# Performance work log

Measured on AMD Instinct MI355X. Metric: run time of the kernel, lower is better.

The kernel has to match this reference:

```python
import jax, jax.numpy as jnp
import numpy as np

H = 4096       # hidden_size
D_IN = 8192    # intermediate_size
N = 16         # ssm_state_size
K = 4          # conv_kernel
R = 256        # time_step_rank
EPS = 1e-6     # mixer_rms_eps


def rms_forward(x, eps=EPS):
    xf = x.astype(jnp.float32)
    var = jnp.mean(xf * xf, axis=-1, keepdims=True)
    return (xf * jax.lax.rsqrt(var + eps)).astype(x.dtype)


def setup_inputs() -> dict:
    key = jax.random.key(0)
    ks = jax.random.split(key, 10)
    s = 0.02
    hidden_states = jax.random.normal(ks[0], (2, 1024, H), dtype=jnp.float32)
    W_in = jax.random.normal(ks[1], (2 * D_IN, H), dtype=jnp.float32) * s
    conv_w = jax.random.normal(ks[2], (D_IN, K), dtype=jnp.float32) * 0.2
    conv_b = jax.random.normal(ks[3], (D_IN,), dtype=jnp.float32) * 0.02
    W_x = jax.random.normal(ks[4], (R + 2 * N, D_IN), dtype=jnp.float32) * s
    W_dt = jax.random.normal(ks[5], (D_IN, R), dtype=jnp.float32) * s
    b_dt = jax.random.normal(ks[6], (D_IN,), dtype=jnp.float32) * 0.02
    A_log = jnp.log(jnp.broadcast_to(jnp.arange(1, N + 1, dtype=jnp.float32)[None, :], (D_IN, N)))
    D = jnp.ones((D_IN,), dtype=jnp.float32)
    W_out = jax.random.normal(ks[7], (H, D_IN), dtype=jnp.float32) * s
    return {"hidden_states": hidden_states, "W_in": W_in, "conv_w": conv_w,
            "conv_b": conv_b, "W_x": W_x, "W_dt": W_dt, "b_dt": b_dt,
            "A_log": A_log, "D": D, "W_out": W_out}


def reference(hidden_states, W_in, conv_w, conv_b, W_x, W_dt, b_dt, A_log, D, W_out):
    b, L, _ = hidden_states.shape
    # in_proj -> split into x and gate  [b, L, d_in] each
    proj = hidden_states @ W_in.T
    x, gate = proj[..., :D_IN], proj[..., D_IN:]
    # depthwise causal conv1d over time (padding K-1, keep first L) + SiLU
    xpad = jnp.pad(x, ((0, 0), (K - 1, 0), (0, 0)))
    xc = conv_b
    for j in range(K):
        xc = xc + conv_w[:, j] * xpad[:, j:j + L, :]
    x = jax.nn.silu(xc)                               # [b, L, d_in]
    # x_proj -> dt / B / C, each RMS-normalized (weightless, FalconMamba)
    ssm = x @ W_x.T                                   # [b, L, R+2N]
    ts, Bm, Cm = ssm[..., :R], ssm[..., R:R + N], ssm[..., R + N:]
    ts = rms_forward(ts)
    Bm = rms_forward(Bm)
    Cm = rms_forward(Cm)
    dt = jax.nn.softplus(ts @ W_dt.T + b_dt)          # [b, L, d_in]
    A = -jnp.exp(A_log.astype(jnp.float32))           # [d_in, N]
    # selective scan over time: state [b, d_in, N]
    def step(state, inp):
        dt_t, B_t, C_t, u_t = inp                     # [b,d],[b,N],[b,N],[b,d]
        dA = jnp.exp(dt_t[..., None] * A)             # [b, d_in, N]
        state = state * dA + (dt_t * u_t)[..., None] * B_t[:, None, :]
        y = jnp.einsum('bdn,bn->bd', state, C_t)
        return state, y
    init = jnp.zeros((b, D_IN, N), dtype=jnp.float32)
    xs = (dt.transpose(1, 0, 2), Bm.transpose(1, 0, 2),
          Cm.transpose(1, 0, 2), x.transpose(1, 0, 2))
    _, ys = jax.lax.scan(step, init, xs)              # [L, b, d_in]
    y = ys.transpose(1, 0, 2) + x * D                 # skip with D
    y = y * jax.nn.silu(gate)                         # gated output
    return y @ W_out.T                                # [b, L, H]
```

## Files before the change

kernel.cpp:

```cpp
#include <hip/hip_runtime.h>
#include <hip/hip_bf16.h>

#define DIN 8192
#define HH 4096
#define BLT 2048
#define LSEQ 1024
#define CL 64
#define NCG 32

typedef unsigned short u16;
typedef __bf16 bf16x8 __attribute__((ext_vector_type(8)));
typedef float f32x4v __attribute__((ext_vector_type(4)));

__device__ __forceinline__ u16 f2b(float f) {
  unsigned u = __float_as_uint(f);
  u += 0x7fff + ((u >> 16) & 1);
  return (u16)(u >> 16);
}
__device__ __forceinline__ float b2f(u16 h) {
  return __uint_as_float(((unsigned)h) << 16);
}

__device__ __forceinline__ void gl_lds16(const u16* g, u16* l) {
  __builtin_amdgcn_global_load_lds(
      (const __attribute__((address_space(1))) void*)g,
      (__attribute__((address_space(3))) void*)l, 16, 0, 0);
}

__device__ __forceinline__ int bsw(int r) { return (r & 3) ^ ((r >> 2) & 3); }

__global__ void cvt_in_kernel(const float* __restrict__ Win, u16* __restrict__ Winb,
                              const float* __restrict__ hs, u16* __restrict__ hsb) {
  const long stride = (long)gridDim.x * blockDim.x * 4;
  const long base = ((long)blockIdx.x * blockDim.x + threadIdx.x) * 4;
  for (long i = base; i < 67108864L; i += stride) {
    f32x4v v = *(const f32x4v*)(Win + i);
    ushort4 o;
    o.x = f2b(v[0]); o.y = f2b(v[1]); o.z = f2b(v[2]); o.w = f2b(v[3]);
    *(ushort4*)(Winb + i) = o;
  }
  for (long i = base; i < 8388608L; i += stride) {
    f32x4v v = *(const f32x4v*)(hs + i);
    ushort4 o;
    o.x = f2b(v[0]); o.y = f2b(v[1]); o.z = f2b(v[2]); o.w = f2b(v[3]);
    *(ushort4*)(hsb + i) = o;
  }
}

__global__ void cvt_weights_kernel(
    const float* __restrict__ Wout, u16* __restrict__ Woutb,
    const float* __restrict__ Wdt, u16* __restrict__ Wdtb,
    const float* __restrict__ Wx, u16* __restrict__ Wxb)
{
  const long stride = (long)gridDim.x * blockDim.x * 4;
  const long base = ((long)blockIdx.x * blockDim.x + threadIdx.x) * 4;
  for (long i = base; i < 33554432L; i += stride) {
    f32x4v v = *(const f32x4v*)(Wout + i);
    ushort4 o;
    o.x = f2b(v[0]); o.y = f2b(v[1]); o.z = f2b(v[2]); o.w = f2b(v[3]);
    *(ushort4*)(Woutb + i) = o;
  }
  for (long i = base; i < 2097152L; i += stride) {
    f32x4v v = *(const f32x4v*)(Wdt + i);
    ushort4 o;
    o.x = f2b(v[0]); o.y = f2b(v[1]); o.z = f2b(v[2]); o.w = f2b(v[3]);
    *(ushort4*)(Wdtb + i) = o;
  }
  for (long i = base; i < (long)512 * DIN; i += stride) {
    ushort4 o;
    if (i < (long)288 * DIN) {
      f32x4v v = *(const f32x4v*)(Wx + i);
      o.x = f2b(v[0]); o.y = f2b(v[1]); o.z = f2b(v[2]); o.w = f2b(v[3]);
    } else {
      o.x = 0; o.y = 0; o.z = 0; o.w = 0;
    }
    *(ushort4*)(Wxb + i) = o;
  }
}

__global__ void add2_kernel(const float* __restrict__ a, const float* __restrict__ b,
                            float* __restrict__ o, long n) {
  long i = ((long)blockIdx.x * blockDim.x + threadIdx.x) * 4;
  long stride = (long)gridDim.x * blockDim.x * 4;
  for (; i < n; i += stride) {
    f32x4v va = *(const f32x4v*)(a + i);
    f32x4v vb = *(const f32x4v*)(b + i);
    *(f32x4v*)(o + i) = va + vb;
  }
}

template<int MODE>
__global__ __launch_bounds__(512, 2) void gemm256(
    const u16* __restrict__ A, const u16* __restrict__ B, void* __restrict__ Cp,
    int M, int N, int Kfull, int Ksub, const float* __restrict__ bias = nullptr)
{
  __shared__ __align__(16) u16 lds[3][2][8192];
  const int tid = threadIdx.x;
  const int lane = tid & 63;
  const int wid = tid >> 6;
  const int wm = wid >> 2;
  const int wn = wid & 3;
  const int fr = lane & 15;
  const int fq = lane >> 4;
  const int fs = fq ^ bsw(fr);

  const int nbx = N >> 8;
  const int cpx = gridDim.x >> 3;
  const int bid = blockIdx.x;
  const int swz = (bid & 7) * cpx + (bid >> 3);
  const long m0 = (long)(swz / nbx) << 8;
  const long n0 = (long)(swz % nbx) << 8;
  const long kbase = (long)blockIdx.y * Ksub;

  const int srow = tid >> 2;
  const int sseg = (tid & 3) ^ bsw(srow);
  const u16* ag0 = A + (m0 + srow) * (long)Kfull + kbase + sseg * 8;
  const u16* ag1 = ag0 + 128 * (long)Kfull;
  const u16* bg0 = B + (n0 + srow) * (long)Kfull + kbase + sseg * 8;
  const u16* bg1 = bg0 + 128 * (long)Kfull;

  auto stageA = [&](int c, int koff) {
    gl_lds16(ag0 + koff, &lds[c][0][tid * 8]);
    gl_lds16(bg0 + koff, &lds[c][1][tid * 8]);
  };
  auto stageB = [&](int c, int koff) {
    gl_lds16(ag1 + koff, &lds[c][0][4096 + tid * 8]);
    gl_lds16(bg1 + koff, &lds[c][1][4096 + tid * 8]);
  };

  const int NT = Ksub >> 5;
  stageA(0, 0); stageB(0, 0);
  stageA(1, 32); stageB(1, 32);
  asm volatile("s_waitcnt vmcnt(4)" ::: "memory");
  __builtin_amdgcn_s_barrier();

  f32x4v acc[8][4];
#pragma unroll
  for (int i = 0; i < 8; ++i)
#pragma unroll
    for (int j = 0; j < 4; ++j) acc[i][j] = (f32x4v){0.f, 0.f, 0.f, 0.f};

  const int aoff = (wm * 128 + fr) * 32 + fs * 8;
  const int boff = (wn * 64 + fr) * 32 + fs * 8;
  bf16x8 af[4], bfg[4], al[4];

  int c = 0, cs = 2;
  for (int t = 0; t < NT; ++t) {
    const u16* Asl = &lds[c][0][0];
    const u16* Bsl = &lds[c][1][0];
    const bool pf = (t + 2 < NT);
#pragma unroll
    for (int mi = 0; mi < 4; ++mi) af[mi] = *(const bf16x8*)(Asl + aoff + mi * 512);
#pragma unroll
    for (int ni = 0; ni < 4; ++ni) bfg[ni] = *(const bf16x8*)(Bsl + boff + ni * 512);
    if (pf) stageA(cs, (t + 2) * 32);
    __builtin_amdgcn_s_barrier();
    asm volatile("s_waitcnt lgkmcnt(0)" ::: "memory");
    __builtin_amdgcn_sched_barrier(0);
    __builtin_amdgcn_s_setprio(1);
#pragma unroll
    for (int mi = 0; mi < 4; ++mi)
#pragma unroll
      for (int ni = 0; ni < 4; ++ni)
        acc[mi][ni] = __builtin_amdgcn_mfma_f32_16x16x32_bf16(af[mi], bfg[ni], acc[mi][ni], 0, 0, 0);
    __builtin_amdgcn_s_setprio(0);
#pragma unroll
    for (int mi = 0; mi < 4; ++mi) al[mi] = *(const bf16x8*)(Asl + aoff + 2048 + mi * 512);
    if (pf) stageB(cs, (t + 2) * 32);
    __builtin_amdgcn_s_barrier();
    asm volatile("s_waitcnt lgkmcnt(0)" ::: "memory");
    __builtin_amdgcn_sched_barrier(0);
    __builtin_amdgcn_s_setprio(1);
#pragma unroll
    for (int mi = 0; mi < 4; ++mi)
#pragma unroll
      for (int ni = 0; ni < 4; ++ni)
        acc[mi + 4][ni] = __builtin_amdgcn_mfma_f32_16x16x32_bf16(al[mi], bfg[ni], acc[mi + 4][ni], 0, 0, 0);
    __builtin_amdgcn_s_setprio(0);
    if (pf) {
      asm volatile("s_waitcnt vmcnt(4)" ::: "memory");
    } else {
      asm volatile("s_waitcnt vmcnt(0)" ::: "memory");
    }
    __builtin_amdgcn_s_barrier();
    c = (c == 2) ? 0 : c + 1;
    cs = (cs == 2) ? 0 : cs + 1;
  }

  float* Cf = (float*)Cp + (size_t)blockIdx.y * M * N;
#pragma unroll
  for (int mi = 0; mi < 8; ++mi) {
#pragma unroll
    for (int ni = 0; ni < 4; ++ni) {
      const long col = n0 + wn * 64 + ni * 16 + fr;
      const long rbase = m0 + wm * 128 + mi * 16 + fq * 4;
#pragma unroll
      for (int r = 0; r < 4; ++r) {
        if constexpr (MODE == 1) {
          ((u16*)Cp)[(rbase + r) * N + col] = f2b(acc[mi][ni][r]);
        } else if constexpr (MODE == 0) {
          Cf[(rbase + r) * N + col] = acc[mi][ni][r];
        } else {
          const float z = acc[mi][ni][r] + bias[rbase + r];
          ((float*)Cp)[(rbase + r) * N + col] = (z > 20.f) ? z : log1pf(__expf(z));
        }
      }
    }
  }
}

__global__ __launch_bounds__(256) void conv_silu_tr_kernel(
    const u16* __restrict__ proj, const float* __restrict__ conv_w,
    const float* __restrict__ conv_b, u16* __restrict__ xb, u16* __restrict__ xT)
{
  __shared__ u16 xt[64][68];
  const int t = threadIdx.x;
  const int tr = t >> 4;
  const int dqi = t & 15;
  const long tok0 = (long)blockIdx.x * 64;
  const int d0 = blockIdx.y * 64;
  const int d = d0 + dqi * 4;
  f32x4v cb = *(const f32x4v*)(conv_b + d);
  f32x4v w0 = *(const f32x4v*)(conv_w + (size_t)(d + 0) * 4);
  f32x4v w1 = *(const f32x4v*)(conv_w + (size_t)(d + 1) * 4);
  f32x4v w2 = *(const f32x4v*)(conv_w + (size_t)(d + 2) * 4);
  f32x4v w3 = *(const f32x4v*)(conv_w + (size_t)(d + 3) * 4);
#pragma unroll
  for (int tt = 0; tt < 4; ++tt) {
    const long tok = tok0 + tr + tt * 16;
    const int l = (int)(tok & (LSEQ - 1));
    float a0 = cb[0], a1 = cb[1], a2 = cb[2], a3 = cb[3];
#pragma unroll
    for (int j = 0; j < 4; ++j) {
      const int lj = l - 3 + j;
      if (lj >= 0) {
        ushort4 xv = *(const ushort4*)(proj + (tok - 3 + j) * 16384 + d);
        a0 = fmaf(w0[j], b2f(xv.x), a0);
        a1 = fmaf(w1[j], b2f(xv.y), a1);
        a2 = fmaf(w2[j], b2f(xv.z), a2);
        a3 = fmaf(w3[j], b2f(xv.w), a3);
      }
    }
    ushort4 o;
    o.x = f2b(a0 / (1.f + __expf(-a0)));
    o.y = f2b(a1 / (1.f + __expf(-a1)));
    o.z = f2b(a2 / (1.f + __expf(-a2)));
    o.w = f2b(a3 / (1.f + __expf(-a3)));
    *(ushort4*)(xb + tok * DIN + d) = o;
    *(ushort4*)(&xt[tr + tt * 16][dqi * 4]) = o;
  }
  __syncthreads();
  const int dl = t >> 2;
  const int tq = t & 3;
  u16 buf[16];
#pragma unroll
  for (int i = 0; i < 16; ++i) buf[i] = xt[tq * 16 + i][dl];
  u16* dst = xT + (size_t)(d0 + dl) * BLT + tok0 + tq * 16;
  *(ushort4*)(dst + 0)  = *(ushort4*)&buf[0];
  *(ushort4*)(dst + 4)  = *(ushort4*)&buf[4];
  *(ushort4*)(dst + 8)  = *(ushort4*)&buf[8];
  *(ushort4*)(dst + 12) = *(ushort4*)&buf[12];
}

__global__ __launch_bounds__(64) void rms_kernel(
    const float* __restrict__ part, u16* __restrict__ tsb,
    float* __restrict__ Bn, float* __restrict__ Cn)
{
  const int tok = blockIdx.x;
  const int lane = threadIdx.x;
  const size_t rowoff = (size_t)tok * 512;
  f32x4v t = (f32x4v){0.f, 0.f, 0.f, 0.f};
#pragma unroll
  for (int s = 0; s < 16; ++s)
    t += *(const f32x4v*)(part + (size_t)s * (BLT * 512) + rowoff + lane * 4);
  float ss = t[0]*t[0] + t[1]*t[1] + t[2]*t[2] + t[3]*t[3];
#pragma unroll
  for (int o = 32; o; o >>= 1) ss += __shfl_xor(ss, o);
  const float sc = rsqrtf(ss * (1.f / 256.f) + 1e-6f);
  ushort4 o4;
  o4.x = f2b(t[0] * sc); o4.y = f2b(t[1] * sc);
  o4.z = f2b(t[2] * sc); o4.w = f2b(t[3] * sc);
  *(ushort4*)(tsb + (size_t)tok * 256 + lane * 4) = o4;

  float v = 0.f;
  if (lane < 32) {
#pragma unroll
    for (int s = 0; s < 16; ++s)
      v += part[(size_t)s * (BLT * 512) + rowoff + 256 + lane];
  }
  float g = v * v;
#pragma unroll
  for (int o = 1; o < 16; o <<= 1) g += __shfl_xor(g, o);
  const float scBC = rsqrtf(g * (1.f / 16.f) + 1e-6f);
  if (lane < 16) Bn[(size_t)tok * 16 + lane] = v * scBC;
  else if (lane < 32) Cn[(size_t)tok * 16 + (lane - 16)] = v * scBC;
}

__global__ __launch_bounds__(256) void scan_p1_kernel(
    const float* __restrict__ dtT, const u16* __restrict__ xT,
    const float* __restrict__ Bn, const float* __restrict__ A_log,
    float* __restrict__ partE, float* __restrict__ partS)
{
  __shared__ float Bsh[CL][16];
  const int tid = threadIdx.x;
  const int chunk = blockIdx.y;
  const int d = blockIdx.x * 64 + (tid >> 2);
  const int ln = tid & 3;
  const int tok0 = chunk * CL;
  {
    const int tt = tid >> 2, q = tid & 3;
    *(f32x4v*)&Bsh[tt][q * 4] = *(const f32x4v*)(Bn + (size_t)(tok0 + tt) * 16 + q * 4);
  }
  __syncthreads();
  float a[4];
#pragma unroll
  for (int j = 0; j < 4; ++j) a[j] = -__expf(A_log[(size_t)d * 16 + ln * 4 + j]);
  float E0 = 1.f, E1 = 1.f, E2 = 1.f, E3 = 1.f;
  float S0 = 0.f, S1 = 0.f, S2 = 0.f, S3 = 0.f;
  const float* dtp = dtT + (size_t)d * BLT + tok0;
  const u16* xp = xT + (size_t)d * BLT + tok0;
  for (int l = 0; l < CL; l += 4) {
    f32x4v dt4 = *(const f32x4v*)(dtp + l);
    ushort4 u4 = *(const ushort4*)(xp + l);
#pragma unroll
    for (int i = 0; i < 4; ++i) {
      const float dt = dt4[i];
      const float u = b2f(((const u16*)&u4)[i]);
      const float dtu = dt * u;
      f32x4v Bv = *(const f32x4v*)&Bsh[l + i][ln * 4];
      const float e0 = __expf(dt * a[0]);
      const float e1 = __expf(dt * a[1]);
      const float e2 = __expf(dt * a[2]);
      const float e3 = __expf(dt * a[3]);
      S0 = fmaf(S0, e0, dtu * Bv[0]); E0 *= e0;
      S1 = fmaf(S1, e1, dtu * Bv[1]); E1 *= e1;
      S2 = fmaf(S2, e2, dtu * Bv[2]); E2 *= e2;
      S3 = fmaf(S3, e3, dtu * Bv[3]); E3 *= e3;
    }
  }
  const size_t off = (size_t)chunk * (DIN * 16) + (size_t)d * 16 + ln * 4;
  f32x4v Ev = {E0, E1, E2, E3}, Sv = {S0, S1, S2, S3};
  *(f32x4v*)(partE + off) = Ev;
  *(f32x4v*)(partS + off) = Sv;
}

__global__ __launch_bounds__(256) void scan_p2_kernel(
    const float* __restrict__ partE, float* __restrict__ partS)
{
  const int dn = blockIdx.x * 256 + threadIdx.x;
  float s = 0.f;
  for (int c = 0; c < NCG; ++c) {
    if ((c & 15) == 0) s = 0.f;
    const size_t off = (size_t)c * (DIN * 16) + dn;
    const float e = partE[off];
    const float ps = partS[off];
    partS[off] = s;
    s = fmaf(e, s, ps);
  }
}

__global__ __launch_bounds__(256) void scan_p3_kernel(
    const float* __restrict__ dtT, const u16* __restrict__ xT,
    const float* __restrict__ Bn, const float* __restrict__ Cn,
    const float* __restrict__ A_log, const float* __restrict__ Dv,
    const float* __restrict__ stateIn, const u16* __restrict__ proj,
    u16* __restrict__ yg)
{
  __shared__ float Bsh[CL][16], Csh[CL][16];
  __shared__ u16 gsh[CL][64], ysh[CL][64];
  const int tid = threadIdx.x;
  const int chunk = blockIdx.y;
  const int d0 = blockIdx.x * 64;
  const int dch = tid >> 2;
  const int d = d0 + dch;
  const int ln = tid & 3;
  const int tok0 = chunk * CL;
  {
    const int tt = tid >> 2, q = tid & 3;
    *(f32x4v*)&Bsh[tt][q * 4] = *(const f32x4v*)(Bn + (size_t)(tok0 + tt) * 16 + q * 4);
    *(f32x4v*)&Csh[tt][q * 4] = *(const f32x4v*)(Cn + (size_t)(tok0 + tt) * 16 + q * 4);
    const u16* grow = proj + (size_t)(tok0 + tt) * 16384 + DIN + d0 + q * 16;
#pragma unroll
    for (int qq = 0; qq < 4; ++qq)
      *(ushort4*)&gsh[tt][q * 16 + qq * 4] = *(const ushort4*)(grow + qq * 4);
  }
  __syncthreads();
  float a[4];
#pragma unroll
  for (int j = 0; j < 4; ++j) a[j] = -__expf(A_log[(size_t)d * 16 + ln * 4 + j]);
  f32x4v sv = *(const f32x4v*)(stateIn + (size_t)chunk * (DIN * 16) + (size_t)d * 16 + ln * 4);
  float S0 = sv[0], S1 = sv[1], S2 = sv[2], S3 = sv[3];
  const float Dd = Dv[d];
  const float* dtp = dtT + (size_t)d * BLT + tok0;
  const u16* xp = xT + (size_t)d * BLT + tok0;
  for (int l = 0; l < CL; l += 4) {
    f32x4v dt4 = *(const f32x4v*)(dtp + l);
    ushort4 u4 = *(const ushort4*)(xp + l);
#pragma unroll
    for (int i = 0; i < 4; ++i) {
      const float dt = dt4[i];
      const float u = b2f(((const u16*)&u4)[i]);
      const float dtu = dt * u;
      f32x4v Bv = *(const f32x4v*)&Bsh[l + i][ln * 4];
      f32x4v Cv = *(const f32x4v*)&Csh[l + i][ln * 4];
      const float e0 = __expf(dt * a[0]);
      const float e1 = __expf(dt * a[1]);
      const float e2 = __expf(dt * a[2]);
      const float e3 = __expf(dt * a[3]);
      float y;
      S0 = fmaf(S0, e0, dtu * Bv[0]); y = S0 * Cv[0];
      S1 = fmaf(S1, e1, dtu * Bv[1]); y = fmaf(S1, Cv[1], y);
      S2 = fmaf(S2, e2, dtu * Bv[2]); y = fmaf(S2, Cv[2], y);
      S3 = fmaf(S3, e3, dtu * Bv[3]); y = fmaf(S3, Cv[3], y);
      y += __shfl_xor(y, 1);
      y += __shfl_xor(y, 2);
      if (ln == 0) {
        const float yt = fmaf(u, Dd, y);
        const float gt = b2f(gsh[l + i][dch]);
        const float sg = gt / (1.f + __expf(-gt));
        ysh[l + i][dch] = f2b(yt * sg);
      }
    }
  }
  __syncthreads();
  {
    const int tt = tid >> 2, q = tid & 3;
    u16* yrow = yg + (size_t)(tok0 + tt) * DIN + d0 + q * 16;
#pragma unroll
    for (int qq = 0; qq < 4; ++qq)
      *(ushort4*)(yrow + qq * 4) = *(ushort4*)&ysh[tt][q * 16 + qq * 4];
  }
}

extern "C" void kernel_launch(void* const* d_in, const int* in_sizes, int n_in,
                              void* d_out, int out_size, void* d_ws, size_t ws_size,
                              hipStream_t stream) {
  const float* hs     = (const float*)d_in[0];
  const float* W_in   = (const float*)d_in[1];
  const float* conv_w = (const float*)d_in[2];
  const float* conv_b = (const float*)d_in[3];
  const float* W_x    = (const float*)d_in[4];
  const float* W_dt   = (const float*)d_in[5];
  const float* b_dt   = (const float*)d_in[6];
  const float* A_log  = (const float*)d_in[7];
  const float* Dv     = (const float*)d_in[8];
  const float* W_out  = (const float*)d_in[9];
  float* out = (float*)d_out;

  char* ws = (char*)d_ws;
  size_t off = 0;
  auto alloc = [&](size_t bytes) -> char* {
    char* p = ws + off;
    off += (bytes + 255) & ~(size_t)255;
    return p;
  };

  u16* W_in_b = (u16*)alloc(134217728);
  u16* hs_b = (u16*)alloc(16777216);
  u16* proj_b = (u16*)alloc((size_t)BLT * 16384 * 2);
  u16* x_b    = (u16*)alloc((size_t)BLT * DIN * 2);
  u16* W_xp_b = (u16*)alloc((size_t)512 * DIN * 2);
  u16* yg_b   = (u16*)alloc((size_t)BLT * DIN * 2);
  u16* x_T    = (u16*)alloc((size_t)BLT * DIN * 2);

  float* dt_T    = (float*)W_in_b;
  float* ssm_part= (float*)W_in_b;
  u16*   W_out_b = (u16*)((char*)W_in_b + 67108864);
  u16*   ts_b    = (u16*)((char*)hs_b + 3145728);
  float* Bn      = (float*)((char*)hs_b + 3145728 + 1048576);
  float* Cn      = (float*)((char*)hs_b + 3145728 + 1048576 + 131072);
  u16*   W_dt_b  = (u16*)((char*)hs_b + 3145728 + 1048576 + 262144);
  float* partE   = (float*)x_b;
  float* partS   = (float*)((char*)x_b + 16777216);
  float* out_part= (float*)proj_b;

  const int CG = 2048;
  cvt_in_kernel<<<CG, 256, 0, stream>>>(W_in, W_in_b, hs, hs_b);
  gemm256<1><<<dim3((16384 / 256) * (BLT / 256), 1), 512, 0, stream>>>(hs_b, W_in_b, proj_b, BLT, 16384, 4096, 4096);
  cvt_weights_kernel<<<CG, 256, 0, stream>>>(W_out, W_out_b, W_dt, W_dt_b, W_x, W_xp_b);
  conv_silu_tr_kernel<<<dim3(BLT / 64, DIN / 64), 256, 0, stream>>>(proj_b, conv_w, conv_b, x_b, x_T);
  gemm256<0><<<dim3((512 / 256) * (BLT / 256), 16), 512, 0, stream>>>(x_b, W_xp_b, ssm_part, BLT, 512, DIN, DIN / 16);
  rms_kernel<<<BLT, 64, 0, stream>>>(ssm_part, ts_b, Bn, Cn);
  gemm256<2><<<dim3((DIN / 256) * (BLT / 256), 1), 512, 0, stream>>>(W_dt_b, ts_b, dt_T, DIN, BLT, 256, 256, b_dt);
  scan_p1_kernel<<<dim3(DIN / 64, NCG), 256, 0, stream>>>(dt_T, x_T, Bn, A_log, partE, partS);
  scan_p2_kernel<<<DIN * 16 / 256, 256, 0, stream>>>(partE, partS);
  scan_p3_kernel<<<dim3(DIN / 64, NCG), 256, 0, stream>>>(dt_T, x_T, Bn, Cn, A_log, Dv, partS, proj_b, yg_b);
  gemm256<0><<<dim3((HH / 256) * (BLT / 256), 2), 512, 0, stream>>>(yg_b, W_out_b, out_part, BLT, HH, DIN, DIN / 2);
  add2_kernel<<<CG, 256, 0, stream>>>(out_part, out_part + (size_t)BLT * HH, out, (long)BLT * HH);
}
```

Before: 897.5 us.

## Replace split-K output GEMM and add kernel with a 256x128 tile GEMM

The final out-projection GEMM previously used split-K=2 with 256x256 tiles, writing two fp32 partial outputs and then summing them in a separate add kernel. It is replaced by a new 256x128-tile GEMM that walks the full K dimension and writes the output directly, which gives the same 256-block grid while removing the partial-buffer traffic and one launch. The x_proj GEMM epilogue also skips storing padded columns beyond 288. The cost is a longer serial K loop per block and a smaller tile that reuses each loaded operand less.

Measured after the change: 888.6 us (median of 2 runs). No clear change (-1.0%).

```diff
diff --git a/kernel.cpp b/kernel.cpp
--- a/kernel.cpp
+++ b/kernel.cpp
@@ -78,21 +78,11 @@
   }
 }
 
-__global__ void add2_kernel(const float* __restrict__ a, const float* __restrict__ b,
-                            float* __restrict__ o, long n) {
-  long i = ((long)blockIdx.x * blockDim.x + threadIdx.x) * 4;
-  long stride = (long)gridDim.x * blockDim.x * 4;
-  for (; i < n; i += stride) {
-    f32x4v va = *(const f32x4v*)(a + i);
-    f32x4v vb = *(const f32x4v*)(b + i);
-    *(f32x4v*)(o + i) = va + vb;
-  }
-}
-
 template<int MODE>
 __global__ __launch_bounds__(512, 2) void gemm256(
     const u16* __restrict__ A, const u16* __restrict__ B, void* __restrict__ Cp,
-    int M, int N, int Kfull, int Ksub, const float* __restrict__ bias = nullptr)
+    int M, int N, int Kfull, int Ksub, const float* __restrict__ bias = nullptr,
+    int nlim = 1 << 30)
 {
   __shared__ __align__(16) u16 lds[3][2][8192];
   const int tid = threadIdx.x;
@@ -199,12 +189,103 @@
         if constexpr (MODE == 1) {
           ((u16*)Cp)[(rbase + r) * N + col] = f2b(acc[mi][ni][r]);
         } else if constexpr (MODE == 0) {
-          Cf[(rbase + r) * N + col] = acc[mi][ni][r];
+          if (col < nlim) Cf[(rbase + r) * N + col] = acc[mi][ni][r];
         } else {
           const float z = acc[mi][ni][r] + bias[rbase + r];
           ((float*)Cp)[(rbase + r) * N + col] = (z > 20.f) ? z : log1pf(__expf(z));
         }
       }
+    }
+  }
+}
+
+__global__ __launch_bounds__(512, 2) void gemm256n128(
+    const u16* __restrict__ A, const u16* __restrict__ B, float* __restrict__ Cp,
+    int M, int N, int K)
+{
+  __shared__ __align__(16) u16 lds[3][12288];
+  const int tid = threadIdx.x;
+  const int lane = tid & 63;
+  const int wid = tid >> 6;
+  const int wm = wid >> 1;
+  const int wn = wid & 1;
+  const int fr = lane & 15;
+  const int fq = lane >> 4;
+  const int fs = fq ^ bsw(fr);
+
+  const int nbx = N >> 7;
+  const int cpx = gridDim.x >> 3;
+  const int bid = blockIdx.x;
+  const int swz = (bid & 7) * cpx + (bid >> 3);
+  const long m0 = (long)(swz / nbx) << 8;
+  const long n0 = (long)(swz % nbx) << 7;
+
+  const int srow = tid >> 2;
+  const int sseg = (tid & 3) ^ bsw(srow);
+  const u16* ag0 = A + (m0 + srow) * (long)K + sseg * 8;
+  const u16* ag1 = ag0 + 128 * (long)K;
+  const u16* bg0 = B + (n0 + srow) * (long)K + sseg * 8;
+
+  auto stage = [&](int c, int koff) {
+    gl_lds16(ag0 + koff, &lds[c][tid * 8]);
+    gl_lds16(ag1 + koff, &lds[c][4096 + tid * 8]);
+    gl_lds16(bg0 + koff, &lds[c][8192 + tid * 8]);
+  };
+
+  const int NT = K >> 5;
+  stage(0, 0);
+  stage(1, 32);
+  asm volatile("s_waitcnt vmcnt(3)" ::: "memory");
+  __builtin_amdgcn_s_barrier();
+
+  f32x4v acc[4][4];
+#pragma unroll
+  for (int i = 0; i < 4; ++i)
+#pragma unroll
+    for (int j = 0; j < 4; ++j) acc[i][j] = (f32x4v){0.f, 0.f, 0.f, 0.f};
+
+  const int aoff = (wm * 64 + fr) * 32 + fs * 8;
+  const int boff = 8192 + (wn * 64 + fr) * 32 + fs * 8;
+  bf16x8 af[4], bfg[4];
+
+  int c = 0, cs = 2;
+  for (int t = 0; t < NT; ++t) {
+    const u16* L = &lds[c][0];
+    const bool pf = (t + 2 < NT);
+#pragma unroll
+    for (int mi = 0; mi < 4; ++mi) af[mi] = *(const bf16x8*)(L + aoff + mi * 512);
+#pragma unroll
+    for (int ni = 0; ni < 4; ++ni) bfg[ni] = *(const bf16x8*)(L + boff + ni * 512);
+    if (pf) stage(cs, (t + 2) * 32);
+    __builtin_amdgcn_s_barrier();
+    asm volatile("s_waitcnt lgkmcnt(0)" ::: "memory");
+    __builtin_amdgcn_sched_barrier(0);
+    __builtin_amdgcn_s_setprio(1);
+#pragma unroll
+    for (int mi = 0; mi < 4; ++mi)
+#pragma unroll
+      for (int ni = 0; ni < 4; ++ni)
+        acc[mi][ni] = __builtin_amdgcn_mfma_f32_16x16x32_bf16(af[mi], bfg[ni], acc[mi][ni], 0, 0, 0);
+    __builtin_amdgcn_s_setprio(0);
+    if (pf) {
+      asm volatile("s_waitcnt vmcnt(3)" ::: "memory");
+    } else {
+      asm volatile("s_waitcnt vmcnt(0)" ::: "memory");
+    }
+    __builtin_amdgcn_s_barrier();
+    c = (c == 2) ? 0 : c + 1;
+    cs = (cs == 2) ? 0 : cs + 1;
+  }
+
+#pragma unroll
+  for (int mi = 0; mi < 4; ++mi) {
+#pragma unroll
+    for (int ni = 0; ni < 4; ++ni) {
+      const long col = n0 + wn * 64 + ni * 16 + fr;
+      const long rbase = m0 + wm * 64 + mi * 16 + fq * 4;
+#pragma unroll
+      for (int r = 0; r < 4; ++r)
+        Cp[(rbase + r) * N + col] = acc[mi][ni][r];
     }
   }
 }
@@ -472,19 +553,17 @@
   u16*   W_dt_b  = (u16*)((char*)hs_b + 3145728 + 1048576 + 262144);
   float* partE   = (float*)x_b;
   float* partS   = (float*)((char*)x_b + 16777216);
-  float* out_part= (float*)proj_b;
 
   const int CG = 2048;
   cvt_in_kernel<<<CG, 256, 0, stream>>>(W_in, W_in_b, hs, hs_b);
   gemm256<1><<<dim3((16384 / 256) * (BLT / 256), 1), 512, 0, stream>>>(hs_b, W_in_b, proj_b, BLT, 16384, 4096, 4096);
   cvt_weights_kernel<<<CG, 256, 0, stream>>>(W_out, W_out_b, W_dt, W_dt_b, W_x, W_xp_b);
   conv_silu_tr_kernel<<<dim3(BLT / 64, DIN / 64), 256, 0, stream>>>(proj_b, conv_w, conv_b, x_b, x_T);
-  gemm256<0><<<dim3((512 / 256) * (BLT / 256), 16), 512, 0, stream>>>(x_b, W_xp_b, ssm_part, BLT, 512, DIN, DIN / 16);
+  gemm256<0><<<dim3((512 / 256) * (BLT / 256), 16), 512, 0, stream>>>(x_b, W_xp_b, ssm_part, BLT, 512, DIN, DIN / 16, nullptr, 288);
   rms_kernel<<<BLT, 64, 0, stream>>>(ssm_part, ts_b, Bn, Cn);
   gemm256<2><<<dim3((DIN / 256) * (BLT / 256), 1), 512, 0, stream>>>(W_dt_b, ts_b, dt_T, DIN, BLT, 256, 256, b_dt);
   scan_p1_kernel<<<dim3(DIN / 64, NCG), 256, 0, stream>>>(dt_T, x_T, Bn, A_log, partE, partS);
   scan_p2_kernel<<<DIN * 16 / 256, 256, 0, stream>>>(partE, partS);
   scan_p3_kernel<<<dim3(DIN / 64, NCG), 256, 0, stream>>>(dt_T, x_T, Bn, Cn, A_log, Dv, partS, proj_b, yg_b);
-  gemm256<0><<<dim3((HH / 256) * (BLT / 256), 2), 512, 0, stream>>>(yg_b, W_out_b, out_part, BLT, HH, DIN, DIN / 2);
-  add2_kernel<<<CG, 256, 0, stream>>>(out_part, out_part + (size_t)BLT * HH, out, (long)BLT * HH);
-}
+  gemm256n128<<<(HH / 128) * (BLT / 256), 512, 0, stream>>>(yg_b, W_out_b, out, BLT, HH, DIN);
+}
```
